# Performance work log

Measured on AMD Instinct MI355X. Metric: run time of the kernel, lower is better.

Reference implementation:

```python
import jax, jax.numpy as jnp
import numpy as np

BETA = 0.25  # args.beta
B, T, D, K = 16, 4096, 64, 1024


def setup_inputs() -> dict:
    key = jax.random.key(0)
    kz, kw = jax.random.split(key)
    z = jax.random.normal(kz, (B, T, D), dtype=jnp.float32)
    # nn.Embedding weight init: uniform(-1/K, 1/K)
    emb = jax.random.uniform(kw, (K, D), dtype=jnp.float32,
                             minval=-1.0 / K, maxval=1.0 / K)
    return {"z": z, "emb": emb}


def reference(z, emb):
    # z: [B, T, D] (torch code loops over first dim; all elements non-empty here)
    # emb: [K, D] codebook
    b, t, d = z.shape
    zf = z.reshape(-1, d)                                   # [B*T, D]
    # squared euclidean distances: ||z||^2 + ||e||^2 - 2 z.e
    dist = (jnp.sum(zf * zf, axis=1, keepdims=True)
            + jnp.sum(emb * emb, axis=1)
            - 2.0 * zf @ emb.T)                             # [B*T, K]
    idx = jnp.argmin(dist, axis=1).reshape(b, t)            # [B, T] int
    z_q_raw = emb[idx]                                      # [B, T, D] gather
    sg = jax.lax.stop_gradient
    # per-batch-element means, summed (loop accumulates loss per z_t)
    commit = jnp.mean((sg(z_q_raw) - z) ** 2, axis=(1, 2))  # [B]
    codebk = jnp.mean((z_q_raw - sg(z)) ** 2, axis=(1, 2))  # [B]
    loss = jnp.sum(BETA * commit + codebk)
    # straight-through estimator
    z_q = z + sg(z_q_raw - z)
    return z_q, loss, idx
```

## Files before the change

### kernel.cpp

```cpp
#include <hip/hip_runtime.h>
#include <math.h>
#include <float.h>

#define NROWS    65536
#define DD       64
#define KK       1024
#define LOSS_OFF 4194304
#define IDX_OFF  4194305
#define RPB      64
#define MAXC     16
#define TPR      4
#define NRND     16

typedef short  short8 __attribute__((ext_vector_type(8)));
typedef float  f32x4  __attribute__((ext_vector_type(4)));

__device__ __forceinline__ void async_copy16(void* lds, const void* g) {
    __builtin_amdgcn_global_load_lds(
        (const __attribute__((address_space(1))) unsigned int*)g,
        (__attribute__((address_space(3))) unsigned int*)lds, 16, 0, 0);
}

__device__ __forceinline__ unsigned short bf16rne(float x) {
    unsigned int u = __float_as_uint(x);
    return (unsigned short)((u + 0x7fffu + ((u >> 16) & 1u)) >> 16);
}

__device__ __forceinline__ float np_sumsq64_stream(const float* p) {
#pragma clang fp contract(off)
    float r[8];
    {
        const float4 u0 = *reinterpret_cast<const float4*>(p);
        const float4 u1 = *reinterpret_cast<const float4*>(p + 4);
        r[0] = u0.x * u0.x; r[1] = u0.y * u0.y; r[2] = u0.z * u0.z; r[3] = u0.w * u0.w;
        r[4] = u1.x * u1.x; r[5] = u1.y * u1.y; r[6] = u1.z * u1.z; r[7] = u1.w * u1.w;
    }
#pragma unroll
    for (int i = 8; i < 64; i += 8) {
        const float4 u0 = *reinterpret_cast<const float4*>(p + i);
        const float4 u1 = *reinterpret_cast<const float4*>(p + i + 4);
        r[0] += u0.x * u0.x; r[1] += u0.y * u0.y; r[2] += u0.z * u0.z; r[3] += u0.w * u0.w;
        r[4] += u1.x * u1.x; r[5] += u1.y * u1.y; r[6] += u1.z * u1.z; r[7] += u1.w * u1.w;
    }
    return ((r[0] + r[1]) + (r[2] + r[3])) + ((r[4] + r[5]) + (r[6] + r[7]));
}

__global__ void vq_prep(const float* __restrict__ emb,
                        float* __restrict__ bn,
                        unsigned short* __restrict__ ebf) {
#pragma clang fp contract(off)
    const int gtid = blockIdx.x * 256 + threadIdx.x;
    const int code = gtid >> 3;
    const int j    = gtid & 7;
    const float* ep = emb + (size_t)code * DD;
    float r = 0.f;
#pragma unroll
    for (int i = 0; i < 8; ++i) {
        const float v = ep[8 * i + j];
        r += v * v;
    }
    const float s1 = r  + __shfl_xor(r,  1, 64);
    const float s2 = s1 + __shfl_xor(s1, 2, 64);
    const float s3 = s2 + __shfl_xor(s2, 4, 64);
    if (j == 0) bn[code] = s3;

    const float* cp = emb + (size_t)gtid * 8;
    const float4 u0 = *reinterpret_cast<const float4*>(cp);
    const float4 u1 = *reinterpret_cast<const float4*>(cp + 4);
    short8 s;
    s[0] = (short)bf16rne(u0.x); s[1] = (short)bf16rne(u0.y);
    s[2] = (short)bf16rne(u0.z); s[3] = (short)bf16rne(u0.w);
    s[4] = (short)bf16rne(u1.x); s[5] = (short)bf16rne(u1.y);
    s[6] = (short)bf16rne(u1.z); s[7] = (short)bf16rne(u1.w);
    *reinterpret_cast<short8*>(ebf + (size_t)gtid * 8) = s;
}

__global__ __launch_bounds__(256)
void vq_main(const float* __restrict__ z, const float* __restrict__ emb,
             const unsigned short* __restrict__ ebf,
             const float* __restrict__ bn, float* __restrict__ out) {
    __shared__ char  dbuf[2][TPR * 2048] __attribute__((aligned(16)));
    __shared__ float a_s[RPB];
    __shared__ float bn_s[KK];
    __shared__ int   cnt[RPB];
    __shared__ int   clist[RPB][MAXC];
    __shared__ int   bidx[RPB];

    const int tid  = threadIdx.x;
    const int lane = tid & 63;
    const int wv   = __builtin_amdgcn_readfirstlane(tid) >> 6;
    const int q    = lane >> 4;
    const int c16  = lane & 15;
    const int rowbase = blockIdx.x * RPB;

    const char* sbase = (const char*)ebf + (size_t)c16 * 128 + (size_t)q * 16;
    char* dst0 = &dbuf[0][wv * 2048 + lane * 16];
    char* dst1 = &dbuf[1][wv * 2048 + lane * 16];

    if (tid < RPB) {
        a_s[tid] = np_sumsq64_stream(z + (size_t)(rowbase + tid) * DD);
        cnt[tid] = 0;
    }
    {
        const int i = tid * 4;
        *reinterpret_cast<float4*>(&bn_s[i]) =
            *reinterpret_cast<const float4*>(bn + i);
    }

    short8 afr[2];
#pragma unroll
    for (int kh = 0; kh < 2; ++kh) {
        const float* zp = z + (size_t)(rowbase + 16 * wv + c16) * DD
                          + 32 * kh + 8 * q;
        const float4 u0 = *reinterpret_cast<const float4*>(zp);
        const float4 u1 = *reinterpret_cast<const float4*>(zp + 4);
        short8 s;
        s[0] = (short)bf16rne(u0.x); s[1] = (short)bf16rne(u0.y);
        s[2] = (short)bf16rne(u0.z); s[3] = (short)bf16rne(u0.w);
        s[4] = (short)bf16rne(u1.x); s[5] = (short)bf16rne(u1.y);
        s[6] = (short)bf16rne(u1.z); s[7] = (short)bf16rne(u1.w);
        afr[kh] = s;
    }

    auto stage = [&](int R, int buf) {
        const char* s0 = sbase + (size_t)(TPR * R + wv) * 2048;
        char* d = buf ? dst1 : dst0;
        async_copy16(d,        s0);
        async_copy16(d + 1024, s0 + 64);
    };

    float mn[4];
#pragma unroll
    for (int i = 0; i < 4; ++i) mn[i] = FLT_MAX;

    stage(0, 0);
    __syncthreads();

    for (int R = 0; R < NRND; ++R) {
        const int cur = R & 1;
        if (R < NRND - 1) stage(R + 1, cur ^ 1);
#pragma unroll
        for (int j = 0; j < TPR; ++j) {
            const char* tb = &dbuf[cur][j * 2048 + lane * 16];
            const short8 b0 = *reinterpret_cast<const short8*>(tb);
            const short8 b1 = *reinterpret_cast<const short8*>(tb + 1024);
            f32x4 acc = {0.f, 0.f, 0.f, 0.f};
            acc = __builtin_amdgcn_mfma_f32_16x16x32_bf16(afr[0], b0, acc, 0, 0, 0);
            acc = __builtin_amdgcn_mfma_f32_16x16x32_bf16(afr[1], b1, acc, 0, 0, 0);
            const float bnv = bn_s[16 * (TPR * R + j) + c16];
#pragma unroll
            for (int r = 0; r < 4; ++r)
                mn[r] = fminf(mn[r], fmaf(-2.f, acc[r], bnv));
        }
        __syncthreads();
    }

#pragma unroll
    for (int mask = 1; mask < 16; mask <<= 1)
#pragma unroll
        for (int i = 0; i < 4; ++i)
            mn[i] = fminf(mn[i], __shfl_xor(mn[i], mask, 64));
    float T[4];
#pragma unroll
    for (int i = 0; i < 4; ++i) {
        const int rowl = 16 * wv + 4 * q + i;
        T[i] = mn[i] + 1.8e-4f * sqrtf(a_s[rowl]) + 1.2e-4f;
    }

    stage(0, 0);
    __syncthreads();

    for (int R = 0; R < NRND; ++R) {
        const int cur = R & 1;
        if (R < NRND - 1) stage(R + 1, cur ^ 1);
#pragma unroll
        for (int j = 0; j < TPR; ++j) {
            const char* tb = &dbuf[cur][j * 2048 + lane * 16];
            const short8 b0 = *reinterpret_cast<const short8*>(tb);
            const short8 b1 = *reinterpret_cast<const short8*>(tb + 1024);
            f32x4 acc = {0.f, 0.f, 0.f, 0.f};
            acc = __builtin_amdgcn_mfma_f32_16x16x32_bf16(afr[0], b0, acc, 0, 0, 0);
            acc = __builtin_amdgcn_mfma_f32_16x16x32_bf16(afr[1], b1, acc, 0, 0, 0);
            const int col = 16 * (TPR * R + j) + c16;
            const float bnv = bn_s[col];
#pragma unroll
            for (int r = 0; r < 4; ++r) {
                const float d0 = fmaf(-2.f, acc[r], bnv);
                if (d0 <= T[r]) {
                    const int rowl = 16 * wv + 4 * q + r;
                    const int slot = atomicAdd(&cnt[rowl], 1);
                    if (slot < MAXC) clist[rowl][slot] = col;
                }
            }
        }
        __syncthreads();
    }

    {
        const int rowl = 16 * wv + c16;
        const int row  = rowbase + rowl;
        const int nc   = cnt[rowl];
        const bool full = nc > MAXC;
        const int lim  = full ? KK : nc;
        const float av = a_s[rowl];
        const float* zp = z + (size_t)row * DD;
        float sb = FLT_MAX;
        int   cb = 0x7fffffff;
        for (int jj = q; jj < lim; jj += 4) {
            const int c = full ? jj : clist[rowl][jj];
            const float* ep = emb + (size_t)c * DD;
            float dot = 0.f;
#pragma unroll
            for (int d = 0; d < DD; d += 4) {
                const float4 zv = *reinterpret_cast<const float4*>(zp + d);
                const float4 ev = *reinterpret_cast<const float4*>(ep + d);
                dot = fmaf(zv.x, ev.x, dot); dot = fmaf(zv.y, ev.y, dot);
                dot = fmaf(zv.z, ev.z, dot); dot = fmaf(zv.w, ev.w, dot);
            }
            const float tt = av + bn_s[c];
            const float sd = fmaf(-2.f, dot, tt);
            if (sd < sb || (sd == sb && c < cb)) { sb = sd; cb = c; }
        }
#pragma unroll
        for (int mask = 16; mask < 64; mask <<= 1) {
            const float so = __shfl_xor(sb, mask, 64);
            const int   co = __shfl_xor(cb, mask, 64);
            if (so < sb || (so == sb && co < cb)) { sb = so; cb = co; }
        }
        if (cb > 1023) cb = 0;
        if (q == 0) bidx[rowl] = cb;
    }
    __syncthreads();

    if (tid >= RPB) return;
    const int row = rowbase + tid;
    const int bid = bidx[tid];
    const float* ep = emb + (size_t)bid * DD;
    const float* zp = z + (size_t)row * DD;
    float* op = out + (size_t)row * DD;
    double sac = 0.0;
#pragma unroll
    for (int d = 0; d < DD; d += 4) {
        const float4 zv = *reinterpret_cast<const float4*>(zp + d);
        const float4 e4 = *reinterpret_cast<const float4*>(ep + d);
        const float df0 = e4.x - zv.x;
        const float df1 = e4.y - zv.y;
        const float df2 = e4.z - zv.z;
        const float df3 = e4.w - zv.w;
        float4 qv;
        qv.x = zv.x + df0; qv.y = zv.y + df1;
        qv.z = zv.z + df2; qv.w = zv.w + df3;
        *reinterpret_cast<float4*>(op + d) = qv;
        sac += (double)(df0 * df0); sac += (double)(df1 * df1);
        sac += (double)(df2 * df2); sac += (double)(df3 * df3);
    }
    out[IDX_OFF + row] = (float)bid;

#pragma unroll
    for (int off = 32; off > 0; off >>= 1) sac += __shfl_down(sac, off, 64);
    if (lane == 0)
        atomicAdd(&out[LOSS_OFF], (float)((1.25 * sac) / 262144.0));
}

extern "C" void kernel_launch(void* const* d_in, const int* in_sizes, int n_in,
                              void* d_out, int out_size, void* d_ws, size_t ws_size,
                              hipStream_t stream) {
    const float* z   = (const float*)d_in[0];
    const float* emb = (const float*)d_in[1];
    float* out = (float*)d_out;

    float*          bnw = (float*)d_ws;
    unsigned short* ebf = (unsigned short*)((char*)d_ws + 4096);

    vq_prep<<<dim3(32), dim3(256), 0, stream>>>(emb, bnw, ebf);
    vq_main<<<dim3(NROWS / RPB), dim3(256), 0, stream>>>(z, emb, ebf, bnw, out);
}
```

Baseline: 126.3 us.

## Fuse two-pass argmin into single pass with running threshold and 32-row waves

Replaces the two full sweeps over the codebook (one to find the minimum distance, one to collect near-minimum candidates) with a single sweep. Candidates are collected against a running per-row minimum that is refreshed after every group of four tiles. LDS double-buffered async staging of the bf16 codebook is dropped: B fragments are read straight from global memory, and each wave now handles two 16-row tiles so every codebook load feeds twice as many MFMAs. The block grows to 128 rows with a minimum occupancy hint of 2. The cost is that early, looser thresholds can admit more candidates, which makes overflow into the slow full-scan fallback more likely.

```diff
diff --git a/kernel.cpp b/kernel.cpp
--- a/kernel.cpp
+++ b/kernel.cpp
@@ -7,19 +7,14 @@
 #define KK       1024
 #define LOSS_OFF 4194304
 #define IDX_OFF  4194305
-#define RPB      64
+#define RPB      128
+#define RW       32
 #define MAXC     16
+#define NT       64
 #define TPR      4
-#define NRND     16
 
 typedef short  short8 __attribute__((ext_vector_type(8)));
 typedef float  f32x4  __attribute__((ext_vector_type(4)));
-
-__device__ __forceinline__ void async_copy16(void* lds, const void* g) {
-    __builtin_amdgcn_global_load_lds(
-        (const __attribute__((address_space(1))) unsigned int*)g,
-        (__attribute__((address_space(3))) unsigned int*)lds, 16, 0, 0);
-}
 
 __device__ __forceinline__ unsigned short bf16rne(float x) {
     unsigned int u = __float_as_uint(x);
@@ -75,11 +70,10 @@
     *reinterpret_cast<short8*>(ebf + (size_t)gtid * 8) = s;
 }
 
-__global__ __launch_bounds__(256)
+__global__ __launch_bounds__(256, 2)
 void vq_main(const float* __restrict__ z, const float* __restrict__ emb,
              const unsigned short* __restrict__ ebf,
              const float* __restrict__ bn, float* __restrict__ out) {
-    __shared__ char  dbuf[2][TPR * 2048] __attribute__((aligned(16)));
     __shared__ float a_s[RPB];
     __shared__ float bn_s[KK];
     __shared__ int   cnt[RPB];
@@ -93,10 +87,6 @@
     const int c16  = lane & 15;
     const int rowbase = blockIdx.x * RPB;
 
-    const char* sbase = (const char*)ebf + (size_t)c16 * 128 + (size_t)q * 16;
-    char* dst0 = &dbuf[0][wv * 2048 + lane * 16];
-    char* dst1 = &dbuf[1][wv * 2048 + lane * 16];
-
     if (tid < RPB) {
         a_s[tid] = np_sumsq64_stream(z + (size_t)(rowbase + tid) * DD);
         cnt[tid] = 0;
@@ -107,97 +97,105 @@
             *reinterpret_cast<const float4*>(bn + i);
     }
 
-    short8 afr[2];
-#pragma unroll
-    for (int kh = 0; kh < 2; ++kh) {
-        const float* zp = z + (size_t)(rowbase + 16 * wv + c16) * DD
-                          + 32 * kh + 8 * q;
-        const float4 u0 = *reinterpret_cast<const float4*>(zp);
-        const float4 u1 = *reinterpret_cast<const float4*>(zp + 4);
-        short8 s;
-        s[0] = (short)bf16rne(u0.x); s[1] = (short)bf16rne(u0.y);
-        s[2] = (short)bf16rne(u0.z); s[3] = (short)bf16rne(u0.w);
-        s[4] = (short)bf16rne(u1.x); s[5] = (short)bf16rne(u1.y);
-        s[6] = (short)bf16rne(u1.z); s[7] = (short)bf16rne(u1.w);
-        afr[kh] = s;
-    }
-
-    auto stage = [&](int R, int buf) {
-        const char* s0 = sbase + (size_t)(TPR * R + wv) * 2048;
-        char* d = buf ? dst1 : dst0;
-        async_copy16(d,        s0);
-        async_copy16(d + 1024, s0 + 64);
-    };
-
-    float mn[4];
-#pragma unroll
-    for (int i = 0; i < 4; ++i) mn[i] = FLT_MAX;
-
-    stage(0, 0);
+    short8 afr[2][2];
+#pragma unroll
+    for (int s = 0; s < 2; ++s)
+#pragma unroll
+        for (int kh = 0; kh < 2; ++kh) {
+            const float* zp = z + (size_t)(rowbase + RW * wv + 16 * s + c16) * DD
+                              + 32 * kh + 8 * q;
+            const float4 u0 = *reinterpret_cast<const float4*>(zp);
+            const float4 u1 = *reinterpret_cast<const float4*>(zp + 4);
+            short8 t;
+            t[0] = (short)bf16rne(u0.x); t[1] = (short)bf16rne(u0.y);
+            t[2] = (short)bf16rne(u0.z); t[3] = (short)bf16rne(u0.w);
+            t[4] = (short)bf16rne(u1.x); t[5] = (short)bf16rne(u1.y);
+            t[6] = (short)bf16rne(u1.z); t[7] = (short)bf16rne(u1.w);
+            afr[s][kh] = t;
+        }
+
     __syncthreads();
 
-    for (int R = 0; R < NRND; ++R) {
-        const int cur = R & 1;
-        if (R < NRND - 1) stage(R + 1, cur ^ 1);
+    float wadd[2][4];
+#pragma unroll
+    for (int s = 0; s < 2; ++s)
+#pragma unroll
+        for (int i = 0; i < 4; ++i) {
+            const int rowl = RW * wv + 16 * s + 4 * q + i;
+            wadd[s][i] = 1.8e-4f * sqrtf(a_s[rowl]) + 1.2e-4f;
+        }
+
+    const short* bb = (const short*)ebf + c16 * 64 + q * 8;
+
+    float mn[2][4];
+#pragma unroll
+    for (int s = 0; s < 2; ++s)
+#pragma unroll
+        for (int i = 0; i < 4; ++i) mn[s][i] = FLT_MAX;
+
+    for (int t0 = 0; t0 < NT; t0 += TPR) {
+        f32x4 dvA[TPR], dvB[TPR];
 #pragma unroll
         for (int j = 0; j < TPR; ++j) {
-            const char* tb = &dbuf[cur][j * 2048 + lane * 16];
+            const short* tb = bb + (size_t)(t0 + j) * 1024;
             const short8 b0 = *reinterpret_cast<const short8*>(tb);
-            const short8 b1 = *reinterpret_cast<const short8*>(tb + 1024);
-            f32x4 acc = {0.f, 0.f, 0.f, 0.f};
-            acc = __builtin_amdgcn_mfma_f32_16x16x32_bf16(afr[0], b0, acc, 0, 0, 0);
-            acc = __builtin_amdgcn_mfma_f32_16x16x32_bf16(afr[1], b1, acc, 0, 0, 0);
-            const float bnv = bn_s[16 * (TPR * R + j) + c16];
-#pragma unroll
-            for (int r = 0; r < 4; ++r)
-                mn[r] = fminf(mn[r], fmaf(-2.f, acc[r], bnv));
-        }
-        __syncthreads();
-    }
-
-#pragma unroll
-    for (int mask = 1; mask < 16; mask <<= 1)
-#pragma unroll
-        for (int i = 0; i < 4; ++i)
-            mn[i] = fminf(mn[i], __shfl_xor(mn[i], mask, 64));
-    float T[4];
-#pragma unroll
-    for (int i = 0; i < 4; ++i) {
-        const int rowl = 16 * wv + 4 * q + i;
-        T[i] = mn[i] + 1.8e-4f * sqrtf(a_s[rowl]) + 1.2e-4f;
-    }
-
-    stage(0, 0);
-    __syncthreads();
-
-    for (int R = 0; R < NRND; ++R) {
-        const int cur = R & 1;
-        if (R < NRND - 1) stage(R + 1, cur ^ 1);
+            const short8 b1 = *reinterpret_cast<const short8*>(tb + 32);
+            f32x4 aA = {0.f, 0.f, 0.f, 0.f};
+            f32x4 aB = {0.f, 0.f, 0.f, 0.f};
+            aA = __builtin_amdgcn_mfma_f32_16x16x32_bf16(afr[0][0], b0, aA, 0, 0, 0);
+            aA = __builtin_amdgcn_mfma_f32_16x16x32_bf16(afr[0][1], b1, aA, 0, 0, 0);
+            aB = __builtin_amdgcn_mfma_f32_16x16x32_bf16(afr[1][0], b0, aB, 0, 0, 0);
+            aB = __builtin_amdgcn_mfma_f32_16x16x32_bf16(afr[1][1], b1, aB, 0, 0, 0);
+            const float bnv = bn_s[16 * (t0 + j) + c16];
+#pragma unroll
+            for (int r = 0; r < 4; ++r) {
+                dvA[j][r] = fmaf(-2.f, aA[r], bnv);
+                dvB[j][r] = fmaf(-2.f, aB[r], bnv);
+            }
+        }
+#pragma unroll
+        for (int j = 0; j < TPR; ++j)
+#pragma unroll
+            for (int r = 0; r < 4; ++r) {
+                mn[0][r] = fminf(mn[0][r], dvA[j][r]);
+                mn[1][r] = fminf(mn[1][r], dvB[j][r]);
+            }
+#pragma unroll
+        for (int mask = 1; mask < 16; mask <<= 1)
+#pragma unroll
+            for (int s = 0; s < 2; ++s)
+#pragma unroll
+                for (int r = 0; r < 4; ++r)
+                    mn[s][r] = fminf(mn[s][r], __shfl_xor(mn[s][r], mask, 64));
+        float thr[2][4];
+#pragma unroll
+        for (int s = 0; s < 2; ++s)
+#pragma unroll
+            for (int r = 0; r < 4; ++r) thr[s][r] = mn[s][r] + wadd[s][r];
 #pragma unroll
         for (int j = 0; j < TPR; ++j) {
-            const char* tb = &dbuf[cur][j * 2048 + lane * 16];
-            const short8 b0 = *reinterpret_cast<const short8*>(tb);
-            const short8 b1 = *reinterpret_cast<const short8*>(tb + 1024);
-            f32x4 acc = {0.f, 0.f, 0.f, 0.f};
-            acc = __builtin_amdgcn_mfma_f32_16x16x32_bf16(afr[0], b0, acc, 0, 0, 0);
-            acc = __builtin_amdgcn_mfma_f32_16x16x32_bf16(afr[1], b1, acc, 0, 0, 0);
-            const int col = 16 * (TPR * R + j) + c16;
-            const float bnv = bn_s[col];
+            const int col = 16 * (t0 + j) + c16;
 #pragma unroll
             for (int r = 0; r < 4; ++r) {
-                const float d0 = fmaf(-2.f, acc[r], bnv);
-                if (d0 <= T[r]) {
-                    const int rowl = 16 * wv + 4 * q + r;
+                if (dvA[j][r] <= thr[0][r]) {
+                    const int rowl = RW * wv + 4 * q + r;
                     const int slot = atomicAdd(&cnt[rowl], 1);
                     if (slot < MAXC) clist[rowl][slot] = col;
                 }
-            }
-        }
-        __syncthreads();
-    }
-
-    {
-        const int rowl = 16 * wv + c16;
+                if (dvB[j][r] <= thr[1][r]) {
+                    const int rowl = RW * wv + 16 + 4 * q + r;
+                    const int slot = atomicAdd(&cnt[rowl], 1);
+                    if (slot < MAXC) clist[rowl][slot] = col;
+                }
+            }
+        }
+    }
+
+    __syncthreads();
+
+#pragma unroll
+    for (int s = 0; s < 2; ++s) {
+        const int rowl = RW * wv + 16 * s + c16;
         const int row  = rowbase + rowl;
         const int nc   = cnt[rowl];
         const bool full = nc > MAXC;
```

New measurement: 286.4 us. 2.27x slower.

## Merge two-pass bf16 candidate search into a single pass with running-min threshold

Applied to the files above, without the earlier changes.

Replaces the separate min-finding pass and candidate-collection pass over the codebook with one pass. Each round computes the distances once, updates a running row minimum via shuffles, and collects candidates against the current threshold. This halves the MFMA work and codebook LDS staging. The running threshold is looser early on, so more candidates get collected and MAXC is raised to 32. Rows that overflow still fall back to a full fp32 scan, and each round adds extra shuffles and atomics.

```diff
diff --git a/kernel.cpp b/kernel.cpp
--- a/kernel.cpp
+++ b/kernel.cpp
@@ -8,7 +8,7 @@
 #define LOSS_OFF 4194304
 #define IDX_OFF  4194305
 #define RPB      64
-#define MAXC     16
+#define MAXC     32
 #define TPR      4
 #define NRND     16
 
@@ -129,16 +129,24 @@
         async_copy16(d + 1024, s0 + 64);
     };
 
-    float mn[4];
-#pragma unroll
-    for (int i = 0; i < 4; ++i) mn[i] = FLT_MAX;
-
     stage(0, 0);
     __syncthreads();
+
+    float wadd[4];
+#pragma unroll
+    for (int i = 0; i < 4; ++i) {
+        const int rowl = 16 * wv + 4 * q + i;
+        wadd[i] = 1.8e-4f * sqrtf(a_s[rowl]) + 1.2e-4f;
+    }
+
+    float mn[4];
+#pragma unroll
+    for (int i = 0; i < 4; ++i) mn[i] = FLT_MAX;
 
     for (int R = 0; R < NRND; ++R) {
         const int cur = R & 1;
         if (R < NRND - 1) stage(R + 1, cur ^ 1);
+        float dv[TPR][4];
 #pragma unroll
         for (int j = 0; j < TPR; ++j) {
             const char* tb = &dbuf[cur][j * 2048 + lane * 16];
@@ -150,43 +158,27 @@
             const float bnv = bn_s[16 * (TPR * R + j) + c16];
 #pragma unroll
             for (int r = 0; r < 4; ++r)
-                mn[r] = fminf(mn[r], fmaf(-2.f, acc[r], bnv));
-        }
-        __syncthreads();
-    }
-
-#pragma unroll
-    for (int mask = 1; mask < 16; mask <<= 1)
-#pragma unroll
-        for (int i = 0; i < 4; ++i)
-            mn[i] = fminf(mn[i], __shfl_xor(mn[i], mask, 64));
-    float T[4];
-#pragma unroll
-    for (int i = 0; i < 4; ++i) {
-        const int rowl = 16 * wv + 4 * q + i;
-        T[i] = mn[i] + 1.8e-4f * sqrtf(a_s[rowl]) + 1.2e-4f;
-    }
-
-    stage(0, 0);
-    __syncthreads();
-
-    for (int R = 0; R < NRND; ++R) {
-        const int cur = R & 1;
-        if (R < NRND - 1) stage(R + 1, cur ^ 1);
+                dv[j][r] = fmaf(-2.f, acc[r], bnv);
+        }
+#pragma unroll
+        for (int j = 0; j < TPR; ++j)
+#pragma unroll
+            for (int r = 0; r < 4; ++r)
+                mn[r] = fminf(mn[r], dv[j][r]);
+#pragma unroll
+        for (int mask = 1; mask < 16; mask <<= 1)
+#pragma unroll
+            for (int r = 0; r < 4; ++r)
+                mn[r] = fminf(mn[r], __shfl_xor(mn[r], mask, 64));
+        float thr[4];
+#pragma unroll
+        for (int r = 0; r < 4; ++r) thr[r] = mn[r] + wadd[r];
 #pragma unroll
         for (int j = 0; j < TPR; ++j) {
-            const char* tb = &dbuf[cur][j * 2048 + lane * 16];
-            const short8 b0 = *reinterpret_cast<const short8*>(tb);
-            const short8 b1 = *reinterpret_cast<const short8*>(tb + 1024);
-            f32x4 acc = {0.f, 0.f, 0.f, 0.f};
-            acc = __builtin_amdgcn_mfma_f32_16x16x32_bf16(afr[0], b0, acc, 0, 0, 0);
-            acc = __builtin_amdgcn_mfma_f32_16x16x32_bf16(afr[1], b1, acc, 0, 0, 0);
             const int col = 16 * (TPR * R + j) + c16;
-            const float bnv = bn_s[col];
 #pragma unroll
             for (int r = 0; r < 4; ++r) {
-                const float d0 = fmaf(-2.f, acc[r], bnv);
-                if (d0 <= T[r]) {
+                if (dv[j][r] <= thr[r]) {
                     const int rowl = 16 * wv + 4 * q + r;
                     const int slot = atomicAdd(&cnt[rowl], 1);
                     if (slot < MAXC) clist[rowl][slot] = col;
```

Measured after the change: 124.2 us. About the same (-1.7%).
